# Kernel tuning notes

Measured on AMD Instinct MI355X. Metric: run time of the kernel, lower is better.

The kernel has to match this reference:

```python
import jax, jax.numpy as jnp
import numpy as np

B, V, D, H, E = 512, 128, 256, 4, 2
Dh = D // H

def setup_inputs() -> dict:
    key = jax.random.key(0)
    k = jax.random.split(key, 8)
    x = jax.random.normal(k[0], (B, V, D), dtype=jnp.float32)
    adj = jax.random.randint(k[1], (V, V), 0, 2, dtype=jnp.int32)
    adj = adj.at[jnp.arange(V), jnp.arange(V)].set(1)  # self loops so no empty columns for real nodes
    edge_attr = jax.random.normal(k[2], (V, V, E), dtype=jnp.float32)
    mask = jax.random.bernoulli(k[3], 0.1, (B, V))  # True = padded view
    # learned params (torch Linear: y = x @ W.T)
    W = jax.random.normal(k[4], (D, D), dtype=jnp.float32) / np.sqrt(D)
    a = jax.random.normal(k[5], (2 * Dh,), dtype=jnp.float32) / np.sqrt(2 * Dh)  # attn.weight flattened
    Ew = jax.random.normal(k[6], (H, E), dtype=jnp.float32) / np.sqrt(E)  # edge_proj.weight
    return {"x": x, "adj": adj, "edge_attr": edge_attr, "mask": mask, "W": W, "a": a, "Ew": Ew}

def reference(x, adj, edge_attr, mask, W, a, Ew):
    Bv, Vv, Dv = x.shape
    Hh = Ew.shape[0]
    Dhh = Dv // Hh
    Wx = (x @ W.T).reshape(Bv, Vv, Hh, Dhh)                 # [B,V,H,Dh]
    a_src, a_dst = a[:Dhh], a[Dhh:]
    s_src = jnp.einsum('bvhd,d->bvh', Wx, a_src)             # a^T[Wh_i ; .]
    s_dst = jnp.einsum('bvhd,d->bvh', Wx, a_dst)             # a^T[. ; Wh_j]
    ef = jnp.einsum('ije,he->ijh', edge_attr, Ew)            # [V,V,H]
    e = s_src[:, :, None, :] + s_dst[:, None, :, :] + ef[None]  # [B,i,j,H]
    e = jnp.where(e >= 0, e, 0.2 * e)                        # leaky_relu(0.2)
    valid = (adj.astype(bool))[None, :, :, None] & (~mask)[:, :, None, None] & (~mask)[:, None, :, None]
    e = jnp.where(valid, e, -jnp.inf)
    # softmax over source dim i (axis=1), safe for all-masked columns (-> 0, like nan_to_num)
    m = jnp.max(e, axis=1, keepdims=True)
    m = jnp.where(jnp.isfinite(m), m, 0.0)
    p = jnp.where(valid, jnp.exp(e - m), 0.0)
    denom = jnp.sum(p, axis=1, keepdims=True)
    alpha = p / jnp.where(denom == 0, 1.0, denom)            # [B,i,j,H]
    h = jnp.einsum('bijh,bihd->bjhd', alpha, Wx).reshape(Bv, Vv, Dv)
    h = jax.nn.elu(h)
    return jnp.where(mask[:, :, None], 0.0, h)
```

## Files before the change

kernel.cpp:

```cpp
#include <hip/hip_runtime.h>
#include <hip/hip_bf16.h>
#include <cmath>

#define BB 512
#define VV 128
#define DD 256
#define HH 4
#define DHH 64

typedef unsigned short u16;
typedef __attribute__((ext_vector_type(8))) short bf16x8;
typedef __attribute__((ext_vector_type(4))) float f32x4;

__device__ __forceinline__ unsigned pk2(float a, float b) {
    __hip_bfloat162 h = __float22bfloat162_rn(make_float2(a, b));
    unsigned r;
    __builtin_memcpy(&r, &h, sizeof(r));
    return r;
}

__global__ __launch_bounds__(256) void k_ef(const float* __restrict__ ea,
                                            const float* __restrict__ Ew,
                                            const int* __restrict__ adj,
                                            float* __restrict__ efmT) {
    __shared__ float tile[32][33];
    const int jt = blockIdx.x, it = blockIdx.y, h = blockIdx.z;
    const int t = threadIdx.x;
    const float e0 = Ew[h * 2], e1 = Ew[h * 2 + 1];
    const int jl = t & 31, il = t >> 5;
    #pragma unroll
    for (int p = 0; p < 4; ++p) {
        const int i = it * 32 + p * 8 + il;
        const int j = jt * 32 + jl;
        const int ij = i * VV + j;
        float v = -INFINITY;
        if (adj[ij]) v = fmaf(ea[ij * 2 + 1], e1, ea[ij * 2] * e0);
        tile[p * 8 + il][jl] = v;
    }
    __syncthreads();
    const int i2 = t & 31, j2 = t >> 5;
    #pragma unroll
    for (int p = 0; p < 4; ++p) {
        const int j = p * 8 + j2;
        efmT[((size_t)h * VV + jt * 32 + j) * VV + it * 32 + i2] = tile[i2][j];
    }
}

__global__ __launch_bounds__(256, 4) void k_fused(
    const float* __restrict__ x, const float* __restrict__ Wm,
    const float* __restrict__ a, const float* __restrict__ efmT,
    const int* __restrict__ mask, float* __restrict__ out) {
    __shared__ u16 ubuf[128 * 136];
    __shared__ float ssl[256], sdl[256], rden[2][128];
    __shared__ int mkl[128];

    u16* As  = ubuf;
    u16* Bs  = ubuf + 128 * 40;
    u16* WxL = ubuf;

    const int t = threadIdx.x;
    const int b = blockIdx.x, hp = blockIdx.y;
    const int w = t >> 6, L = t & 63;
    const int wr = w >> 1, wc = w & 1;
    const int lr = L & 15, lg = L >> 4;

    if (t < 128) mkl[t] = mask[b * VV + t];

    const int row = t >> 1, seg = t & 1;
    const float* xs = x  + ((size_t)b * VV + row) * DD + seg * 16;
    const float* ws = Wm + ((size_t)(hp * 128 + row)) * DD + seg * 16;
    u16* adst = As + row * 40 + seg * 16;
    u16* bdst = Bs + row * 40 + seg * 16;

    f32x4 acc[4][4];
    #pragma unroll
    for (int i = 0; i < 4; ++i)
        #pragma unroll
        for (int j = 0; j < 4; ++j) acc[i][j] = (f32x4){0.f, 0.f, 0.f, 0.f};

    float4 px[4];
    #pragma unroll
    for (int q = 0; q < 4; ++q)
        px[q] = *(const float4*)(xs + q * 4);

    for (int ks = 0; ks < 8; ++ks) {
        float4 qw[4];
        #pragma unroll
        for (int q = 0; q < 4; ++q)
            qw[q] = *(const float4*)(ws + ks * 32 + q * 4);
        unsigned va[4], vb[4], qa[4], qb[4];
        va[0] = pk2(px[0].x, px[0].y); va[1] = pk2(px[0].z, px[0].w);
        va[2] = pk2(px[1].x, px[1].y); va[3] = pk2(px[1].z, px[1].w);
        vb[0] = pk2(px[2].x, px[2].y); vb[1] = pk2(px[2].z, px[2].w);
        vb[2] = pk2(px[3].x, px[3].y); vb[3] = pk2(px[3].z, px[3].w);
        *(bf16x8*)adst       = *(bf16x8*)&va[0];
        *(bf16x8*)(adst + 8) = *(bf16x8*)&vb[0];
        qa[0] = pk2(qw[0].x, qw[0].y); qa[1] = pk2(qw[0].z, qw[0].w);
        qa[2] = pk2(qw[1].x, qw[1].y); qa[3] = pk2(qw[1].z, qw[1].w);
        qb[0] = pk2(qw[2].x, qw[2].y); qb[1] = pk2(qw[2].z, qw[2].w);
        qb[2] = pk2(qw[3].x, qw[3].y); qb[3] = pk2(qw[3].z, qw[3].w);
        *(bf16x8*)bdst       = *(bf16x8*)&qa[0];
        *(bf16x8*)(bdst + 8) = *(bf16x8*)&qb[0];
        __syncthreads();
        if (ks < 7) {
            #pragma unroll
            for (int q = 0; q < 4; ++q)
                px[q] = *(const float4*)(xs + (ks + 1) * 32 + q * 4);
        }
        bf16x8 af[4], bfr[4];
        #pragma unroll
        for (int mi = 0; mi < 4; ++mi)
            af[mi] = *(const bf16x8*)&As[(wr * 64 + mi * 16 + lr) * 40 + lg * 8];
        #pragma unroll
        for (int ni = 0; ni < 4; ++ni)
            bfr[ni] = *(const bf16x8*)&Bs[(wc * 64 + ni * 16 + lr) * 40 + lg * 8];
        #pragma unroll
        for (int mi = 0; mi < 4; ++mi)
            #pragma unroll
            for (int ni = 0; ni < 4; ++ni)
                acc[mi][ni] = __builtin_amdgcn_mfma_f32_16x16x32_bf16(
                    af[mi], bfr[ni], acc[mi][ni], 0, 0, 0);
        __syncthreads();
    }

    float as_[4], ad_[4];
    #pragma unroll
    for (int ni = 0; ni < 4; ++ni) {
        as_[ni] = a[ni * 16 + lr];
        ad_[ni] = a[64 + ni * 16 + lr];
    }
    float ps[16], pd[16];
    #pragma unroll
    for (int k = 0; k < 16; ++k) { ps[k] = 0.f; pd[k] = 0.f; }
    #pragma unroll
    for (int mi = 0; mi < 4; ++mi) {
        #pragma unroll
        for (int ni = 0; ni < 4; ++ni) {
            const int c  = wc * 64 + ni * 16 + lr;
            const int vb = wr * 64 + mi * 16 + lg * 4;
            unsigned o2[2];
            o2[0] = pk2(acc[mi][ni][0], acc[mi][ni][1]);
            o2[1] = pk2(acc[mi][ni][2], acc[mi][ni][3]);
            #pragma unroll
            for (int r = 0; r < 4; ++r) {
                float v = acc[mi][ni][r];
                ps[mi * 4 + r] = fmaf(v, as_[ni], ps[mi * 4 + r]);
                pd[mi * 4 + r] = fmaf(v, ad_[ni], pd[mi * 4 + r]);
            }
            *(uint2*)&WxL[c * 136 + vb] = *(uint2*)&o2[0];
        }
    }
    #pragma unroll
    for (int k = 0; k < 16; ++k) {
        #pragma unroll
        for (int m = 1; m < 16; m <<= 1) {
            ps[k] += __shfl_xor(ps[k], m);
            pd[k] += __shfl_xor(pd[k], m);
        }
    }
    if (lr == 0) {
        #pragma unroll
        for (int mi = 0; mi < 4; ++mi)
            #pragma unroll
            for (int r = 0; r < 4; ++r) {
                int v = wr * 64 + mi * 16 + lg * 4 + r;
                bool mk = mkl[v] != 0;
                ssl[wc * 128 + v] = mk ? -INFINITY : ps[mi * 4 + r];
                sdl[wc * 128 + v] = mk ? -INFINITY : pd[mi * 4 + r];
            }
    }
    __syncthreads();

    const int j0 = w * 32 + lr;
    for (int hl = 0; hl < 2; ++hl) {
        const int h = hp * 2 + hl;
        const float sdj0 = sdl[hl * 128 + j0];
        const float sdj1 = sdl[hl * 128 + j0 + 16];
        const float* ef0 = efmT + ((size_t)h * VV + j0) * VV;
        const float* ef1 = ef0 + 16 * VV;
        bf16x8 af2[2][4];
        float ps0 = 0.f, ps1 = 0.f;
        #pragma unroll
        for (int ks = 0; ks < 4; ++ks) {
            const int i0 = ks * 32 + lg * 8;
            float sv[8], ev0[8], ev1[8];
            *(float4*)&sv[0]  = *(const float4*)&ssl[hl * 128 + i0];
            *(float4*)&sv[4]  = *(const float4*)&ssl[hl * 128 + i0 + 4];
            *(float4*)&ev0[0] = *(const float4*)(ef0 + i0);
            *(float4*)&ev0[4] = *(const float4*)(ef0 + i0 + 4);
            *(float4*)&ev1[0] = *(const float4*)(ef1 + i0);
            *(float4*)&ev1[4] = *(const float4*)(ef1 + i0 + 4);
            float p0[8], p1[8];
            #pragma unroll
            for (int u = 0; u < 8; ++u) {
                float e0 = sv[u] + sdj0 + ev0[u];
                float e1 = sv[u] + sdj1 + ev1[u];
                e0 = fmaxf(e0, 0.2f * e0);
                e1 = fmaxf(e1, 0.2f * e1);
                p0[u] = __expf(e0); ps0 += p0[u];
                p1[u] = __expf(e1); ps1 += p1[u];
            }
            unsigned* a0 = (unsigned*)&af2[0][ks];
            unsigned* a1 = (unsigned*)&af2[1][ks];
            a0[0] = pk2(p0[0], p0[1]); a0[1] = pk2(p0[2], p0[3]);
            a0[2] = pk2(p0[4], p0[5]); a0[3] = pk2(p0[6], p0[7]);
            a1[0] = pk2(p1[0], p1[1]); a1[1] = pk2(p1[2], p1[3]);
            a1[2] = pk2(p1[4], p1[5]); a1[3] = pk2(p1[6], p1[7]);
        }
        ps0 += __shfl_xor(ps0, 16); ps0 += __shfl_xor(ps0, 32);
        ps1 += __shfl_xor(ps1, 16); ps1 += __shfl_xor(ps1, 32);
        if (lg == 0) {
            rden[hl][j0]      = ps0 > 0.f ? 1.f / ps0 : 0.f;
            rden[hl][j0 + 16] = ps1 > 0.f ? 1.f / ps1 : 0.f;
        }

        f32x4 acc2[2][4];
        #pragma unroll
        for (int mi = 0; mi < 2; ++mi)
            #pragma unroll
            for (int ni = 0; ni < 4; ++ni) acc2[mi][ni] = (f32x4){0.f, 0.f, 0.f, 0.f};
        #pragma unroll
        for (int ks = 0; ks < 4; ++ks) {
            const int kk = ks * 32 + lg * 8;
            #pragma unroll
            for (int ni = 0; ni < 4; ++ni) {
                bf16x8 bf2 = *(const bf16x8*)&WxL[(hl * 64 + ni * 16 + lr) * 136 + kk];
                acc2[0][ni] = __builtin_amdgcn_mfma_f32_16x16x32_bf16(
                    af2[0][ks], bf2, acc2[0][ni], 0, 0, 0);
                acc2[1][ni] = __builtin_amdgcn_mfma_f32_16x16x32_bf16(
                    af2[1][ks], bf2, acc2[1][ni], 0, 0, 0);
            }
        }

        #pragma unroll
        for (int mi = 0; mi < 2; ++mi)
            #pragma unroll
            for (int ni = 0; ni < 4; ++ni) {
                const int dcol = ni * 16 + lr;
                const int jb   = w * 32 + mi * 16 + lg * 4;
                float* op = out + ((size_t)b * VV + jb) * DD + h * DHH + dcol;
                #pragma unroll
                for (int r = 0; r < 4; ++r) {
                    float v = acc2[mi][ni][r] * rden[hl][jb + r];
                    v = v > 0.f ? v : (__expf(v) - 1.0f);
                    op[(size_t)r * DD] = v;
                }
            }
    }
}

extern "C" void kernel_launch(void* const* d_in, const int* in_sizes, int n_in,
                              void* d_out, int out_size, void* d_ws, size_t ws_size,
                              hipStream_t stream) {
    const float* x    = (const float*)d_in[0];
    const int*   adj  = (const int*)d_in[1];
    const float* ea   = (const float*)d_in[2];
    const int*   mask = (const int*)d_in[3];
    const float* Wm   = (const float*)d_in[4];
    const float* a    = (const float*)d_in[5];
    const float* Ew   = (const float*)d_in[6];
    float* out = (float*)d_out;

    float* efmT = (float*)d_ws;

    k_ef<<<dim3(4, 4, HH), 256, 0, stream>>>(ea, Ew, adj, efmT);
    k_fused<<<dim3(BB, 2), 256, 0, stream>>>(x, Wm, a, efmT, mask, out);
}
```

Before: 154.3 us.

## Split fused GAT kernel into separate GEMM and attention kernels via workspace

Splits the single fused kernel into a projection GEMM kernel and an attention kernel. The GEMM kernel writes the bf16 transposed Wx and the masked source/destination scores to global workspace, and the attention kernel reads them back from global memory instead of LDS. This removes the large LDS buffer, so more blocks may fit per CU. The cost is an extra launch and a global round trip of roughly 32 MB of bf16 intermediates plus the score arrays. The old fused kernel remains as a fallback when the workspace is too small.

```diff
diff --git a/kernel.cpp b/kernel.cpp
--- a/kernel.cpp
+++ b/kernel.cpp
@@ -46,25 +46,18 @@
     }
 }
 
-__global__ __launch_bounds__(256, 4) void k_fused(
+__global__ __launch_bounds__(256, 4) void k_gemm(
     const float* __restrict__ x, const float* __restrict__ Wm,
-    const float* __restrict__ a, const float* __restrict__ efmT,
-    const int* __restrict__ mask, float* __restrict__ out) {
-    __shared__ u16 ubuf[128 * 136];
-    __shared__ float ssl[256], sdl[256], rden[2][128];
-    __shared__ int mkl[128];
-
-    u16* As  = ubuf;
-    u16* Bs  = ubuf + 128 * 40;
-    u16* WxL = ubuf;
+    const float* __restrict__ a, const int* __restrict__ mask,
+    u16* __restrict__ wxT, float* __restrict__ ssg, float* __restrict__ sdg) {
+    __shared__ u16 As[128 * 40];
+    __shared__ u16 Bs[128 * 40];
 
     const int t = threadIdx.x;
     const int b = blockIdx.x, hp = blockIdx.y;
     const int w = t >> 6, L = t & 63;
     const int wr = w >> 1, wc = w & 1;
     const int lr = L & 15, lg = L >> 4;
-
-    if (t < 128) mkl[t] = mask[b * VV + t];
 
     const int row = t >> 1, seg = t & 1;
     const float* xs = x  + ((size_t)b * VV + row) * DD + seg * 16;
@@ -147,6 +140,225 @@
                 ps[mi * 4 + r] = fmaf(v, as_[ni], ps[mi * 4 + r]);
                 pd[mi * 4 + r] = fmaf(v, ad_[ni], pd[mi * 4 + r]);
             }
+            u16* gw = wxT + ((size_t)(b * 256 + hp * 128 + c)) * 128 + vb;
+            *(uint2*)gw = *(uint2*)&o2[0];
+        }
+    }
+    #pragma unroll
+    for (int k = 0; k < 16; ++k) {
+        #pragma unroll
+        for (int m = 1; m < 16; m <<= 1) {
+            ps[k] += __shfl_xor(ps[k], m);
+            pd[k] += __shfl_xor(pd[k], m);
+        }
+    }
+    if (lr == 0) {
+        const size_t so = (size_t)(b * 4 + hp * 2 + wc) * 128;
+        #pragma unroll
+        for (int mi = 0; mi < 4; ++mi)
+            #pragma unroll
+            for (int r = 0; r < 4; ++r) {
+                int v = wr * 64 + mi * 16 + lg * 4 + r;
+                bool mk = mask[b * VV + v] != 0;
+                ssg[so + v] = mk ? -INFINITY : ps[mi * 4 + r];
+                sdg[so + v] = mk ? -INFINITY : pd[mi * 4 + r];
+            }
+    }
+}
+
+__global__ __launch_bounds__(256, 4) void k_attn(
+    const u16* __restrict__ wxT, const float* __restrict__ ssg,
+    const float* __restrict__ sdg, const float* __restrict__ efmT,
+    float* __restrict__ out) {
+    const int t = threadIdx.x;
+    const int b = blockIdx.x, hp = blockIdx.y;
+    const int w = t >> 6, L = t & 63;
+    const int lr = L & 15, lg = L >> 4;
+
+    const int j0 = w * 32 + lr;
+    for (int hl = 0; hl < 2; ++hl) {
+        const int h = hp * 2 + hl;
+        const float* ssp = ssg + (size_t)(b * 4 + hp * 2 + hl) * 128;
+        const float* sdp = sdg + (size_t)(b * 4 + hp * 2 + hl) * 128;
+        const float sdj0 = sdp[j0];
+        const float sdj1 = sdp[j0 + 16];
+        const float* ef0 = efmT + ((size_t)h * VV + j0) * VV;
+        const float* ef1 = ef0 + 16 * VV;
+        bf16x8 af2[2][4];
+        float ps0 = 0.f, ps1 = 0.f;
+        #pragma unroll
+        for (int ks = 0; ks < 4; ++ks) {
+            const int i0 = ks * 32 + lg * 8;
+            float sv[8], ev0[8], ev1[8];
+            *(float4*)&sv[0]  = *(const float4*)(ssp + i0);
+            *(float4*)&sv[4]  = *(const float4*)(ssp + i0 + 4);
+            *(float4*)&ev0[0] = *(const float4*)(ef0 + i0);
+            *(float4*)&ev0[4] = *(const float4*)(ef0 + i0 + 4);
+            *(float4*)&ev1[0] = *(const float4*)(ef1 + i0);
+            *(float4*)&ev1[4] = *(const float4*)(ef1 + i0 + 4);
+            float p0[8], p1[8];
+            #pragma unroll
+            for (int u = 0; u < 8; ++u) {
+                float e0 = sv[u] + sdj0 + ev0[u];
+                float e1 = sv[u] + sdj1 + ev1[u];
+                e0 = fmaxf(e0, 0.2f * e0);
+                e1 = fmaxf(e1, 0.2f * e1);
+                p0[u] = __expf(e0); ps0 += p0[u];
+                p1[u] = __expf(e1); ps1 += p1[u];
+            }
+            unsigned* a0 = (unsigned*)&af2[0][ks];
+            unsigned* a1 = (unsigned*)&af2[1][ks];
+            a0[0] = pk2(p0[0], p0[1]); a0[1] = pk2(p0[2], p0[3]);
+            a0[2] = pk2(p0[4], p0[5]); a0[3] = pk2(p0[6], p0[7]);
+            a1[0] = pk2(p1[0], p1[1]); a1[1] = pk2(p1[2], p1[3]);
+            a1[2] = pk2(p1[4], p1[5]); a1[3] = pk2(p1[6], p1[7]);
+        }
+        ps0 += __shfl_xor(ps0, 16); ps0 += __shfl_xor(ps0, 32);
+        ps1 += __shfl_xor(ps1, 16); ps1 += __shfl_xor(ps1, 32);
+        const float rdv0 = ps0 > 0.f ? 1.f / ps0 : 0.f;
+        const float rdv1 = ps1 > 0.f ? 1.f / ps1 : 0.f;
+
+        f32x4 acc2[2][4];
+        #pragma unroll
+        for (int mi = 0; mi < 2; ++mi)
+            #pragma unroll
+            for (int ni = 0; ni < 4; ++ni) acc2[mi][ni] = (f32x4){0.f, 0.f, 0.f, 0.f};
+        const u16* wb = wxT + ((size_t)(b * 256 + hp * 128 + hl * 64 + lr)) * 128;
+        #pragma unroll
+        for (int ks = 0; ks < 4; ++ks) {
+            const int kk = ks * 32 + lg * 8;
+            #pragma unroll
+            for (int ni = 0; ni < 4; ++ni) {
+                bf16x8 bf2 = *(const bf16x8*)(wb + (size_t)(ni * 16) * 128 + kk);
+                acc2[0][ni] = __builtin_amdgcn_mfma_f32_16x16x32_bf16(
+                    af2[0][ks], bf2, acc2[0][ni], 0, 0, 0);
+                acc2[1][ni] = __builtin_amdgcn_mfma_f32_16x16x32_bf16(
+                    af2[1][ks], bf2, acc2[1][ni], 0, 0, 0);
+            }
+        }
+
+        #pragma unroll
+        for (int mi = 0; mi < 2; ++mi) {
+            float rd[4];
+            #pragma unroll
+            for (int r = 0; r < 4; ++r)
+                rd[r] = __shfl(mi == 0 ? rdv0 : rdv1, lg * 4 + r, 16);
+            #pragma unroll
+            for (int ni = 0; ni < 4; ++ni) {
+                const int dcol = ni * 16 + lr;
+                const int jb   = w * 32 + mi * 16 + lg * 4;
+                float* op = out + ((size_t)b * VV + jb) * DD + h * DHH + dcol;
+                #pragma unroll
+                for (int r = 0; r < 4; ++r) {
+                    float v = acc2[mi][ni][r] * rd[r];
+                    v = v > 0.f ? v : (__expf(v) - 1.0f);
+                    op[(size_t)r * DD] = v;
+                }
+            }
+        }
+    }
+}
+
+__global__ __launch_bounds__(256, 4) void k_fused(
+    const float* __restrict__ x, const float* __restrict__ Wm,
+    const float* __restrict__ a, const float* __restrict__ efmT,
+    const int* __restrict__ mask, float* __restrict__ out) {
+    __shared__ u16 ubuf[128 * 136];
+    __shared__ float ssl[256], sdl[256], rden[2][128];
+    __shared__ int mkl[128];
+
+    u16* As  = ubuf;
+    u16* Bs  = ubuf + 128 * 40;
+    u16* WxL = ubuf;
+
+    const int t = threadIdx.x;
+    const int b = blockIdx.x, hp = blockIdx.y;
+    const int w = t >> 6, L = t & 63;
+    const int wr = w >> 1, wc = w & 1;
+    const int lr = L & 15, lg = L >> 4;
+
+    if (t < 128) mkl[t] = mask[b * VV + t];
+
+    const int row = t >> 1, seg = t & 1;
+    const float* xs = x  + ((size_t)b * VV + row) * DD + seg * 16;
+    const float* ws = Wm + ((size_t)(hp * 128 + row)) * DD + seg * 16;
+    u16* adst = As + row * 40 + seg * 16;
+    u16* bdst = Bs + row * 40 + seg * 16;
+
+    f32x4 acc[4][4];
+    #pragma unroll
+    for (int i = 0; i < 4; ++i)
+        #pragma unroll
+        for (int j = 0; j < 4; ++j) acc[i][j] = (f32x4){0.f, 0.f, 0.f, 0.f};
+
+    float4 px[4];
+    #pragma unroll
+    for (int q = 0; q < 4; ++q) px[q] = *(const float4*)(xs + q * 4);
+
+    for (int ks = 0; ks < 8; ++ks) {
+        float4 qw[4];
+        #pragma unroll
+        for (int q = 0; q < 4; ++q)
+            qw[q] = *(const float4*)(ws + ks * 32 + q * 4);
+        unsigned va[4], vb[4], qa[4], qb[4];
+        va[0] = pk2(px[0].x, px[0].y); va[1] = pk2(px[0].z, px[0].w);
+        va[2] = pk2(px[1].x, px[1].y); va[3] = pk2(px[1].z, px[1].w);
+        vb[0] = pk2(px[2].x, px[2].y); vb[1] = pk2(px[2].z, px[2].w);
+        vb[2] = pk2(px[3].x, px[3].y); vb[3] = pk2(px[3].z, px[3].w);
+        *(bf16x8*)adst       = *(bf16x8*)&va[0];
+        *(bf16x8*)(adst + 8) = *(bf16x8*)&vb[0];
+        qa[0] = pk2(qw[0].x, qw[0].y); qa[1] = pk2(qw[0].z, qw[0].w);
+        qa[2] = pk2(qw[1].x, qw[1].y); qa[3] = pk2(qw[1].z, qw[1].w);
+        qb[0] = pk2(qw[2].x, qw[2].y); qb[1] = pk2(qw[2].z, qw[2].w);
+        qb[2] = pk2(qw[3].x, qw[3].y); qb[3] = pk2(qw[3].z, qw[3].w);
+        *(bf16x8*)bdst       = *(bf16x8*)&qa[0];
+        *(bf16x8*)(bdst + 8) = *(bf16x8*)&qb[0];
+        __syncthreads();
+        if (ks < 7) {
+            #pragma unroll
+            for (int q = 0; q < 4; ++q)
+                px[q] = *(const float4*)(xs + (ks + 1) * 32 + q * 4);
+        }
+        bf16x8 af[4], bfr[4];
+        #pragma unroll
+        for (int mi = 0; mi < 4; ++mi)
+            af[mi] = *(const bf16x8*)&As[(wr * 64 + mi * 16 + lr) * 40 + lg * 8];
+        #pragma unroll
+        for (int ni = 0; ni < 4; ++ni)
+            bfr[ni] = *(const bf16x8*)&Bs[(wc * 64 + ni * 16 + lr) * 40 + lg * 8];
+        #pragma unroll
+        for (int mi = 0; mi < 4; ++mi)
+            #pragma unroll
+            for (int ni = 0; ni < 4; ++ni)
+                acc[mi][ni] = __builtin_amdgcn_mfma_f32_16x16x32_bf16(
+                    af[mi], bfr[ni], acc[mi][ni], 0, 0, 0);
+        __syncthreads();
+    }
+
+    float as_[4], ad_[4];
+    #pragma unroll
+    for (int ni = 0; ni < 4; ++ni) {
+        as_[ni] = a[ni * 16 + lr];
+        ad_[ni] = a[64 + ni * 16 + lr];
+    }
+    float ps[16], pd[16];
+    #pragma unroll
+    for (int k = 0; k < 16; ++k) { ps[k] = 0.f; pd[k] = 0.f; }
+    #pragma unroll
+    for (int mi = 0; mi < 4; ++mi) {
+        #pragma unroll
+        for (int ni = 0; ni < 4; ++ni) {
+            const int c  = wc * 64 + ni * 16 + lr;
+            const int vb = wr * 64 + mi * 16 + lg * 4;
+            unsigned o2[2];
+            o2[0] = pk2(acc[mi][ni][0], acc[mi][ni][1]);
+            o2[1] = pk2(acc[mi][ni][2], acc[mi][ni][3]);
+            #pragma unroll
+            for (int r = 0; r < 4; ++r) {
+                float v = acc[mi][ni][r];
+                ps[mi * 4 + r] = fmaf(v, as_[ni], ps[mi * 4 + r]);
+                pd[mi * 4 + r] = fmaf(v, ad_[ni], pd[mi * 4 + r]);
+            }
             *(uint2*)&WxL[c * 136 + vb] = *(uint2*)&o2[0];
         }
     }
@@ -213,7 +425,6 @@
             rden[hl][j0]      = ps0 > 0.f ? 1.f / ps0 : 0.f;
             rden[hl][j0 + 16] = ps1 > 0.f ? 1.f / ps1 : 0.f;
         }
-
         f32x4 acc2[2][4];
         #pragma unroll
         for (int mi = 0; mi < 2; ++mi)
@@ -231,7 +442,6 @@
                     af2[1][ks], bf2, acc2[1][ni], 0, 0, 0);
             }
         }
-
         #pragma unroll
         for (int mi = 0; mi < 2; ++mi)
             #pragma unroll
@@ -261,8 +471,22 @@
     const float* Ew   = (const float*)d_in[6];
     float* out = (float*)d_out;
 
-    float* efmT = (float*)d_ws;
+    char* ws = (char*)d_ws;
+    float* efmT = (float*)ws;
+    const size_t EFM_SZ = (size_t)HH * VV * VV * 4;
+    const size_t WXT_SZ = (size_t)BB * 256 * 128 * 2;
+    const size_t SS_SZ  = (size_t)BB * 4 * 128 * 4;
+    const size_t NEED   = EFM_SZ + WXT_SZ + 2 * SS_SZ;
 
     k_ef<<<dim3(4, 4, HH), 256, 0, stream>>>(ea, Ew, adj, efmT);
-    k_fused<<<dim3(BB, 2), 256, 0, stream>>>(x, Wm, a, efmT, mask, out);
-}
+
+    if (ws_size >= NEED) {
+        u16*   wxT = (u16*)(ws + EFM_SZ);
+        float* ssg = (float*)(ws + EFM_SZ + WXT_SZ);
+        float* sdg = (float*)(ws + EFM_SZ + WXT_SZ + SS_SZ);
+        k_gemm<<<dim3(BB, 2), 256, 0, stream>>>(x, Wm, a, mask, wxT, ssg, sdg);
+        k_attn<<<dim3(BB, 2), 256, 0, stream>>>(wxT, ssg, sdg, efmT, out);
+    } else {
+        k_fused<<<dim3(BB, 2), 256, 0, stream>>>(x, Wm, a, efmT, mask, out);
+    }
+}
```

After: 186.6 us. +21.0%, slower.
